# Performance work log

Hardware: AMD Instinct MI355X
Metric: run time of the kernel (lower is better)

## Reference

```python
import jax, jax.numpy as jnp
import numpy as np

MAX_LEN = 150
DIM_HEAD = 64


def setup_inputs() -> dict:
    key = jax.random.key(0)
    kq, kk, kv, kp, km = jax.random.split(key, 5)
    B, H, L, Dh = 4, 16, 1024, DIM_HEAD
    q = jax.random.normal(kq, (B, H, L, Dh), dtype=jnp.float32)
    k = jax.random.normal(kk, (B, H, L, Dh), dtype=jnp.float32)
    v = jax.random.normal(kv, (B, H, L, Dh), dtype=jnp.float32)
    pos_embedding = jax.random.normal(kp, (2 * MAX_LEN + 1, Dh), dtype=jnp.float32)
    mask = jax.random.randint(km, (B, 1, 1, L), 0, 2).astype(bool)
    return {"q": q, "k": k, "v": v, "pos_embedding": pos_embedding, "mask": mask}


def reference(q, k, v, pos_embedding, mask):
    B, H, Lq, Dh = q.shape
    Lk = k.shape[2]
    scale = jnp.asarray(np.sqrt(Dh), dtype=q.dtype)
    # relative position index: clamp(j - i, -max_len, max_len) + max_len - 1
    # (faithful to source, incl. the -1 offset; index -1 wraps to last row in both torch and jax)
    rel = jnp.arange(Lk)[None, :] - jnp.arange(Lq)[:, None]
    rel_idx = jnp.clip(rel, -MAX_LEN, MAX_LEN) + MAX_LEN - 1  # [Lq, Lk]
    R = pos_embedding[rel_idx]  # [Lq, Lk, Dh]
    # relative-position score: q_t @ R^T  ->  [B, H, Lq, Lk]
    rp = jnp.einsum('bhqd,qkd->bhqk', q, R)
    scores = (jnp.einsum('bhqd,bhkd->bhqk', q, k) + rp) / scale
    scores = jnp.where(mask, -jnp.inf, scores)
    attn = jax.nn.softmax(scores, axis=-1)
    return jnp.einsum('bhqk,bhkd->bhqd', attn, v)
```

## Files before the change

kernel.cpp:

```cpp
#include <hip/hip_runtime.h>
#include <math.h>


#define LL 1024
#define DH 64
#define MAXL 150

typedef __attribute__((ext_vector_type(8)))  short    short8;
typedef __attribute__((ext_vector_type(4)))  float    f32x4;
typedef __attribute__((ext_vector_type(16))) float    f32x16;
typedef __attribute__((ext_vector_type(4)))  unsigned u32x4;

union U4S8 { u32x4 u; short8 s; };

__device__ __forceinline__ unsigned f2bf(float f) {
  unsigned u = __float_as_uint(f);
  u += 0x7FFFu + ((u >> 16) & 1u);
  return u >> 16;
}
__device__ __forceinline__ unsigned pkbf(float lo, float hi) {
  return f2bf(lo) | (f2bf(hi) << 16);
}
__device__ __forceinline__ float bf2f(unsigned short s) {
  return __uint_as_float((unsigned)s << 16);
}
__device__ __forceinline__ short8 pack8f(float4 a, float4 b) {
  U4S8 t;
  t.u[0] = pkbf(a.x, a.y); t.u[1] = pkbf(a.z, a.w);
  t.u[2] = pkbf(b.x, b.y); t.u[3] = pkbf(b.z, b.w);
  return t.s;
}
__device__ __forceinline__ int swz(int row, int cb) {
  return row * 128 + (cb ^ ((row & 7) << 4));
}
__device__ __forceinline__ void st_pair(unsigned char* base, int row, int colb,
                                        float a, float b) {
  unsigned u = pkbf(a, b);
  *(unsigned short*)(base + swz(row, colb))     = (unsigned short)u;
  *(unsigned short*)(base + swz(row + 1, colb)) = (unsigned short)(u >> 16);
}
#define KOFF(r) ((((r) & 3)) + 8 * ((r) >> 2))

__global__ __launch_bounds__(256, 2)
void rp_attn32(const float* __restrict__ Q, const float* __restrict__ K,
               const float* __restrict__ V, const float* __restrict__ POS,
               const int* __restrict__ MSK, float* __restrict__ OUT) {
  __shared__ __attribute__((aligned(16))) unsigned short qrs[64][306];
  __shared__ __attribute__((aligned(16))) unsigned char  kv[32768];
  __shared__ __attribute__((aligned(16))) float          mskf[2][64];

  const int tid = threadIdx.x;
  const int F  = blockIdx.x;
  const int gi = F >> 3;
  const int bh = (F & 7) * 8 + (gi >> 4);
  const int i0 = (gi & 15) * 64;
  const int b  = bh >> 4;

  const int wave = tid >> 6, lane = tid & 63;
  const int lo5 = lane & 31, hi = lane >> 5;
  const int qg = wave & 1, kh = wave >> 1;
  const int qloc = qg * 32 + lo5;
  const int irow = i0 + qloc;

  const size_t bo = (size_t)bh * LL * DH;
  const float* qp = Q + bo;
  const float* kp = K + bo;
  const float* vp = V + bo;
  const int*   mrow = MSK + b * LL;

  unsigned char* ksh = kv + kh * 8192;
  unsigned char* vth = kv + 16384 + kh * 8192;

  short8 qB[4];
#pragma unroll
  for (int c = 0; c < 4; ++c) {
    const float* src = qp + (size_t)irow * DH + c * 16 + hi * 8;
    qB[c] = pack8f(*(const float4*)src, *(const float4*)(src + 4));
  }

  for (int tb = kh; tb < 10; tb += 2) {
    int trow = tb * 32 + lo5; if (trow > 300) trow = 300;
    const float* pr = POS + (size_t)trow * DH;
    f32x16 z;
#pragma unroll
    for (int x = 0; x < 16; ++x) z[x] = 0.f;
#pragma unroll
    for (int c = 0; c < 4; ++c) {
      const float* s2 = pr + c * 16 + hi * 8;
      short8 af = pack8f(*(const float4*)s2, *(const float4*)(s2 + 4));
      z = __builtin_amdgcn_mfma_f32_32x32x16_bf16(af, qB[c], z, 0, 0, 0);
    }
#pragma unroll
    for (int rp = 0; rp < 8; ++rp) {
      const int r = rp * 2;
      int tp = KOFF(r) + 4 * hi + 32 * tb;
      if (tp < 306)
        *(unsigned*)(&qrs[qloc][tp]) = pkbf(z[r], z[r + 1]);
    }
  }

  const float SC = 0.18033688011112042f;
  float m2 = -1e30f, lsum = 0.f;
  f32x16 acc0, acc1;
#pragma unroll
  for (int x = 0; x < 16; ++x) { acc0[x] = 0.f; acc1[x] = 0.f; }

  for (int rd = 0; rd < 8; ++rd) {
    __syncthreads();
    {
      const int r = tid >> 2, q4 = tid & 3, r2 = r * 2, rb = q4 * 16;
#pragma unroll
      for (int h = 0; h < 2; ++h) {
        const int j0h = h * 512 + rd * 64;
        const float* ksrc = kp + (size_t)(j0h + r) * DH + q4 * 16;
        float4 k0 = ((const float4*)ksrc)[0], k1 = ((const float4*)ksrc)[1];
        float4 k2 = ((const float4*)ksrc)[2], k3 = ((const float4*)ksrc)[3];
        unsigned char* kb_ = kv + h * 8192;
        *(short8*)(kb_ + swz(r, q4 * 32))      = pack8f(k0, k1);
        *(short8*)(kb_ + swz(r, q4 * 32 + 16)) = pack8f(k2, k3);
        const float* vsrc = vp + (size_t)(j0h + r) * DH + q4 * 16;
        float4 v0 = ((const float4*)vsrc)[0], v1 = ((const float4*)vsrc)[1];
        float4 v2 = ((const float4*)vsrc)[2], v3 = ((const float4*)vsrc)[3];
        unsigned char* vb_ = kv + 16384 + h * 8192;
        st_pair(vb_, rb + 0,  r2, v0.x, v0.y); st_pair(vb_, rb + 2,  r2, v0.z, v0.w);
        st_pair(vb_, rb + 4,  r2, v1.x, v1.y); st_pair(vb_, rb + 6,  r2, v1.z, v1.w);
        st_pair(vb_, rb + 8,  r2, v2.x, v2.y); st_pair(vb_, rb + 10, r2, v2.z, v2.w);
        st_pair(vb_, rb + 12, r2, v3.x, v3.y); st_pair(vb_, rb + 14, r2, v3.z, v3.w);
      }
      if (tid < 128) {
        int h = tid >> 6, kk = tid & 63;
        mskf[h][kk] = mrow[h * 512 + rd * 64 + kk] ? -INFINITY : 0.0f;
      }
    }
    __syncthreads();

    const int j0 = kh * 512 + rd * 64;

    f32x16 st[2];
#pragma unroll
    for (int kb = 0; kb < 2; ++kb) {
      f32x16 z;
#pragma unroll
      for (int x = 0; x < 16; ++x) z[x] = 0.f;
#pragma unroll
      for (int c = 0; c < 4; ++c) {
        short8 kf = *(const short8*)(ksh + swz(kb * 32 + lo5, c * 32 + hi * 16));
        z = __builtin_amdgcn_mfma_f32_32x32x16_bf16(kf, qB[c], z, 0, 0, 0);
      }
      st[kb] = z;
    }

#pragma unroll
    for (int kb = 0; kb < 2; ++kb) {
      const int jb = j0 + kb * 32;
      f32x4 mg[4];
#pragma unroll
      for (int g4 = 0; g4 < 4; ++g4)
        mg[g4] = *(const f32x4*)&mskf[kh][kb * 32 + g4 * 8 + 4 * hi];
      const int relmin = jb - (i0 + qg * 32 + 31);
      const int relmax = jb + 31 - (i0 + qg * 32);
      if (relmin >= MAXL) {
        const float bias = bf2f(qrs[qloc][299]);
#pragma unroll
        for (int r = 0; r < 16; ++r)
          st[kb][r] = (st[kb][r] + bias) * SC + mg[r >> 2][r & 3];
      } else if (relmax <= -MAXL) {
        const float bias = bf2f(qrs[qloc][300]);
#pragma unroll
        for (int r = 0; r < 16; ++r)
          st[kb][r] = (st[kb][r] + bias) * SC + mg[r >> 2][r & 3];
      } else {
#pragma unroll
        for (int r = 0; r < 16; ++r) {
          const int rel = jb + KOFF(r) + 4 * hi - irow;
          const int idx = rel <= -MAXL ? 300 : (rel >= MAXL ? 299 : rel + MAXL - 1);
          st[kb][r] = (st[kb][r] + bf2f(qrs[qloc][idx])) * SC + mg[r >> 2][r & 3];
        }
      }
    }

    f32x16 mx;
#pragma unroll
    for (int r = 0; r < 16; ++r) mx[r] = fmaxf(st[0][r], st[1][r]);
#pragma unroll
    for (int w = 8; w > 0; w >>= 1)
#pragma unroll
      for (int r = 0; r < 8; ++r)
        if (r < w) mx[r] = fmaxf(mx[r], mx[r + w]);
    float tmax = fmaxf(mx[0], __shfl_xor(mx[0], 32));
    const float mnew = fmaxf(m2, tmax);
    const float alpha = exp2f(m2 - mnew);
#pragma unroll
    for (int kb = 0; kb < 2; ++kb)
#pragma unroll
      for (int r = 0; r < 16; ++r) st[kb][r] = exp2f(st[kb][r] - mnew);
    f32x16 sx;
#pragma unroll
    for (int r = 0; r < 16; ++r) sx[r] = st[0][r] + st[1][r];
#pragma unroll
    for (int w = 8; w > 0; w >>= 1)
#pragma unroll
      for (int r = 0; r < 8; ++r)
        if (r < w) sx[r] = sx[r] + sx[r + w];
    const float ps = sx[0] + __shfl_xor(sx[0], 32);
    lsum = lsum * alpha + ps;
    m2 = mnew;
    acc0 *= alpha; acc1 *= alpha;

    short8 pf[4];
#pragma unroll
    for (int ch = 0; ch < 4; ++ch) {
      const int kb = ch >> 1, rb2 = (ch & 1) * 8;
      unsigned a  = pkbf(st[kb][rb2 + 0], st[kb][rb2 + 1]);
      unsigned a2 = pkbf(st[kb][rb2 + 2], st[kb][rb2 + 3]);
      unsigned bb = pkbf(st[kb][rb2 + 4], st[kb][rb2 + 5]);
      unsigned b2 = pkbf(st[kb][rb2 + 6], st[kb][rb2 + 7]);
      unsigned sa  = __shfl_xor(a, 32);
      unsigned sa2 = __shfl_xor(a2, 32);
      unsigned sbb = __shfl_xor(bb, 32);
      unsigned sb2 = __shfl_xor(b2, 32);
      U4S8 t;
      t.u[0] = hi ? sbb : a;
      t.u[1] = hi ? sb2 : a2;
      t.u[2] = hi ? bb  : sa;
      t.u[3] = hi ? b2  : sa2;
      pf[ch] = t.s;
    }

#pragma unroll
    for (int ch = 0; ch < 4; ++ch) {
      short8 vf0 = *(const short8*)(vth + swz(lo5,      ch * 32 + hi * 16));
      short8 vf1 = *(const short8*)(vth + swz(32 + lo5, ch * 32 + hi * 16));
      acc0 = __builtin_amdgcn_mfma_f32_32x32x16_bf16(vf0, pf[ch], acc0, 0, 0, 0);
      acc1 = __builtin_amdgcn_mfma_f32_32x32x16_bf16(vf1, pf[ch], acc1, 0, 0, 0);
    }
  }

  __syncthreads();
  float* mb = (float*)kv;
  if (wave >= 2) {
    float* d = mb + ((wave - 2) * 64 + lane) * 37;
    d[0] = m2; d[1] = lsum;
#pragma unroll
    for (int r = 0; r < 16; ++r) { d[2 + r] = acc0[r]; d[18 + r] = acc1[r]; }
  }
  __syncthreads();
  if (wave < 2) {
    const float* d = mb + (wave * 64 + lane) * 37;
    const float m1 = d[0], l1 = d[1];
    const float mf = fmaxf(m2, m1);
    const float a0 = exp2f(m2 - mf), a1 = exp2f(m1 - mf);
    const float lf = lsum * a0 + l1 * a1;
    const float inv = 1.f / lf;
    float* op = OUT + bo + (size_t)irow * DH;
#pragma unroll
    for (int r = 0; r < 16; ++r) {
      const int d0 = KOFF(r) + 4 * hi;
      op[d0]      = (acc0[r] * a0 + d[2 + r]  * a1) * inv;
      op[d0 + 32] = (acc1[r] * a0 + d[18 + r] * a1) * inv;
    }
  }
}

extern "C" void kernel_launch(void* const* d_in, const int* in_sizes, int n_in,
                              void* d_out, int out_size, void* d_ws, size_t ws_size,
                              hipStream_t stream) {
  const float* q   = (const float*)d_in[0];
  const float* k   = (const float*)d_in[1];
  const float* v   = (const float*)d_in[2];
  const float* pos = (const float*)d_in[3];
  const int*   msk = (const int*)d_in[4];
  float* out = (float*)d_out;

  rp_attn32<<<dim3(1024), dim3(256), 0, stream>>>(q, k, v, pos, msk, out);
}
```

Baseline: 98.67 us.

## Prefetch K/V into registers, use hardware bf16 pack, lazy softmax rescale

Several changes land together. The next K/V tile is loaded from global memory into registers right after the barrier, so the load overlaps the current tile's compute. Software bf16 rounding is replaced with the v_cvt_pk_bf16_f32 instruction. The whole mask row is preloaded into LDS once, and the V transpose store uses a different thread mapping. The online-softmax rescale is skipped unless the running max grows by more than a threshold. In exchange the prefetch adds register pressure, which may hurt occupancy under launch_bounds(256,2), and the lazy rescale leaves probabilities bounded by 2^12 rather than 1 before the bf16 pack.

```diff
diff --git a/kernel.cpp b/kernel.cpp
--- a/kernel.cpp
+++ b/kernel.cpp
@@ -13,21 +13,18 @@
 
 union U4S8 { u32x4 u; short8 s; };
 
-__device__ __forceinline__ unsigned f2bf(float f) {
-  unsigned u = __float_as_uint(f);
-  u += 0x7FFFu + ((u >> 16) & 1u);
-  return u >> 16;
-}
-__device__ __forceinline__ unsigned pkbf(float lo, float hi) {
-  return f2bf(lo) | (f2bf(hi) << 16);
+__device__ __forceinline__ unsigned cvtpk(float lo, float hi) {
+  unsigned r;
+  asm("v_cvt_pk_bf16_f32 %0, %1, %2" : "=v"(r) : "v"(lo), "v"(hi));
+  return r;
 }
 __device__ __forceinline__ float bf2f(unsigned short s) {
   return __uint_as_float((unsigned)s << 16);
 }
 __device__ __forceinline__ short8 pack8f(float4 a, float4 b) {
   U4S8 t;
-  t.u[0] = pkbf(a.x, a.y); t.u[1] = pkbf(a.z, a.w);
-  t.u[2] = pkbf(b.x, b.y); t.u[3] = pkbf(b.z, b.w);
+  t.u[0] = cvtpk(a.x, a.y); t.u[1] = cvtpk(a.z, a.w);
+  t.u[2] = cvtpk(b.x, b.y); t.u[3] = cvtpk(b.z, b.w);
   return t.s;
 }
 __device__ __forceinline__ int swz(int row, int cb) {
@@ -35,7 +32,7 @@
 }
 __device__ __forceinline__ void st_pair(unsigned char* base, int row, int colb,
                                         float a, float b) {
-  unsigned u = pkbf(a, b);
+  unsigned u = cvtpk(a, b);
   *(unsigned short*)(base + swz(row, colb))     = (unsigned short)u;
   *(unsigned short*)(base + swz(row + 1, colb)) = (unsigned short)(u >> 16);
 }
@@ -47,7 +44,7 @@
                const int* __restrict__ MSK, float* __restrict__ OUT) {
   __shared__ __attribute__((aligned(16))) unsigned short qrs[64][306];
   __shared__ __attribute__((aligned(16))) unsigned char  kv[32768];
-  __shared__ __attribute__((aligned(16))) float          mskf[2][64];
+  __shared__ __attribute__((aligned(16))) float          mskf[1024];
 
   const int tid = threadIdx.x;
   const int F  = blockIdx.x;
@@ -62,6 +59,9 @@
   const int qloc = qg * 32 + lo5;
   const int irow = i0 + qloc;
 
+  const int rK = tid >> 2, q4 = tid & 3;
+  const int kkV = tid & 63, dwV = wave;
+
   const size_t bo = (size_t)bh * LL * DH;
   const float* qp = Q + bo;
   const float* kp = K + bo;
@@ -78,6 +78,12 @@
     qB[c] = pack8f(*(const float4*)src, *(const float4*)(src + 4));
   }
 
+#pragma unroll
+  for (int t2 = 0; t2 < 4; ++t2) {
+    const int ix = tid + t2 * 256;
+    mskf[ix] = mrow[ix] ? -INFINITY : 0.0f;
+  }
+
   for (int tb = kh; tb < 10; tb += 2) {
     int trow = tb * 32 + lo5; if (trow > 300) trow = 300;
     const float* pr = POS + (size_t)trow * DH;
@@ -95,7 +101,7 @@
       const int r = rp * 2;
       int tp = KOFF(r) + 4 * hi + 32 * tb;
       if (tp < 306)
-        *(unsigned*)(&qrs[qloc][tp]) = pkbf(z[r], z[r + 1]);
+        *(unsigned*)(&qrs[qloc][tp]) = cvtpk(z[r], z[r + 1]);
     }
   }
 
@@ -105,34 +111,40 @@
 #pragma unroll
   for (int x = 0; x < 16; ++x) { acc0[x] = 0.f; acc1[x] = 0.f; }
 
+  float4 kreg[2][4], vreg[2][4];
+  auto LOADT = [&](int rdx) {
+#pragma unroll
+    for (int h = 0; h < 2; ++h) {
+      const float* ksrc = kp + (size_t)(h * 512 + rdx * 64 + rK) * DH + q4 * 16;
+#pragma unroll
+      for (int i = 0; i < 4; ++i) kreg[h][i] = ((const float4*)ksrc)[i];
+      const float* vsrc = vp + (size_t)(h * 512 + rdx * 64 + kkV) * DH + dwV * 16;
+#pragma unroll
+      for (int i = 0; i < 4; ++i) vreg[h][i] = ((const float4*)vsrc)[i];
+    }
+  };
+  LOADT(0);
+
   for (int rd = 0; rd < 8; ++rd) {
     __syncthreads();
-    {
-      const int r = tid >> 2, q4 = tid & 3, r2 = r * 2, rb = q4 * 16;
-#pragma unroll
-      for (int h = 0; h < 2; ++h) {
-        const int j0h = h * 512 + rd * 64;
-        const float* ksrc = kp + (size_t)(j0h + r) * DH + q4 * 16;
-        float4 k0 = ((const float4*)ksrc)[0], k1 = ((const float4*)ksrc)[1];
-        float4 k2 = ((const float4*)ksrc)[2], k3 = ((const float4*)ksrc)[3];
-        unsigned char* kb_ = kv + h * 8192;
-        *(short8*)(kb_ + swz(r, q4 * 32))      = pack8f(k0, k1);
-        *(short8*)(kb_ + swz(r, q4 * 32 + 16)) = pack8f(k2, k3);
-        const float* vsrc = vp + (size_t)(j0h + r) * DH + q4 * 16;
-        float4 v0 = ((const float4*)vsrc)[0], v1 = ((const float4*)vsrc)[1];
-        float4 v2 = ((const float4*)vsrc)[2], v3 = ((const float4*)vsrc)[3];
-        unsigned char* vb_ = kv + 16384 + h * 8192;
-        st_pair(vb_, rb + 0,  r2, v0.x, v0.y); st_pair(vb_, rb + 2,  r2, v0.z, v0.w);
-        st_pair(vb_, rb + 4,  r2, v1.x, v1.y); st_pair(vb_, rb + 6,  r2, v1.z, v1.w);
-        st_pair(vb_, rb + 8,  r2, v2.x, v2.y); st_pair(vb_, rb + 10, r2, v2.z, v2.w);
-        st_pair(vb_, rb + 12, r2, v3.x, v3.y); st_pair(vb_, rb + 14, r2, v3.z, v3.w);
-      }
-      if (tid < 128) {
-        int h = tid >> 6, kk = tid & 63;
-        mskf[h][kk] = mrow[h * 512 + rd * 64 + kk] ? -INFINITY : 0.0f;
-      }
+#pragma unroll
+    for (int h = 0; h < 2; ++h) {
+      unsigned char* kb_ = kv + h * 8192;
+      *(short8*)(kb_ + swz(rK, q4 * 32))      = pack8f(kreg[h][0], kreg[h][1]);
+      *(short8*)(kb_ + swz(rK, q4 * 32 + 16)) = pack8f(kreg[h][2], kreg[h][3]);
+      unsigned char* vb_ = kv + 16384 + h * 8192;
+      const int db = dwV * 16, cb2 = kkV * 2;
+      st_pair(vb_, db + 0,  cb2, vreg[h][0].x, vreg[h][0].y);
+      st_pair(vb_, db + 2,  cb2, vreg[h][0].z, vreg[h][0].w);
+      st_pair(vb_, db + 4,  cb2, vreg[h][1].x, vreg[h][1].y);
+      st_pair(vb_, db + 6,  cb2, vreg[h][1].z, vreg[h][1].w);
+      st_pair(vb_, db + 8,  cb2, vreg[h][2].x, vreg[h][2].y);
+      st_pair(vb_, db + 10, cb2, vreg[h][2].z, vreg[h][2].w);
+      st_pair(vb_, db + 12, cb2, vreg[h][3].x, vreg[h][3].y);
+      st_pair(vb_, db + 14, cb2, vreg[h][3].z, vreg[h][3].w);
     }
     __syncthreads();
+    if (rd < 7) LOADT(rd + 1);
 
     const int j0 = kh * 512 + rd * 64;
 
@@ -156,7 +168,7 @@
       f32x4 mg[4];
 #pragma unroll
       for (int g4 = 0; g4 < 4; ++g4)
-        mg[g4] = *(const f32x4*)&mskf[kh][kb * 32 + g4 * 8 + 4 * hi];
+        mg[g4] = *(const f32x4*)&mskf[jb + g4 * 8 + 4 * hi];
       const int relmin = jb - (i0 + qg * 32 + 31);
       const int relmax = jb + 31 - (i0 + qg * 32);
       if (relmin >= MAXL) {
@@ -187,13 +199,18 @@
 #pragma unroll
       for (int r = 0; r < 8; ++r)
         if (r < w) mx[r] = fmaxf(mx[r], mx[r + w]);
-    float tmax = fmaxf(mx[0], __shfl_xor(mx[0], 32));
-    const float mnew = fmaxf(m2, tmax);
-    const float alpha = exp2f(m2 - mnew);
+    const float tmax = fmaxf(mx[0], __shfl_xor(mx[0], 32));
+    if (!__all(tmax - m2 <= 12.0f)) {
+      const float mnew = fmaxf(m2, tmax);
+      const float alpha = exp2f(m2 - mnew);
+      lsum *= alpha;
+      acc0 *= alpha; acc1 *= alpha;
+      m2 = mnew;
+    }
 #pragma unroll
     for (int kb = 0; kb < 2; ++kb)
 #pragma unroll
-      for (int r = 0; r < 16; ++r) st[kb][r] = exp2f(st[kb][r] - mnew);
+      for (int r = 0; r < 16; ++r) st[kb][r] = exp2f(st[kb][r] - m2);
     f32x16 sx;
 #pragma unroll
     for (int r = 0; r < 16; ++r) sx[r] = st[0][r] + st[1][r];
@@ -202,19 +219,16 @@
 #pragma unroll
       for (int r = 0; r < 8; ++r)
         if (r < w) sx[r] = sx[r] + sx[r + w];
-    const float ps = sx[0] + __shfl_xor(sx[0], 32);
-    lsum = lsum * alpha + ps;
-    m2 = mnew;
-    acc0 *= alpha; acc1 *= alpha;
+    lsum += sx[0] + __shfl_xor(sx[0], 32);
 
     short8 pf[4];
 #pragma unroll
     for (int ch = 0; ch < 4; ++ch) {
       const int kb = ch >> 1, rb2 = (ch & 1) * 8;
-      unsigned a  = pkbf(st[kb][rb2 + 0], st[kb][rb2 + 1]);
-      unsigned a2 = pkbf(st[kb][rb2 + 2], st[kb][rb2 + 3]);
-      unsigned bb = pkbf(st[kb][rb2 + 4], st[kb][rb2 + 5]);
-      unsigned b2 = pkbf(st[kb][rb2 + 6], st[kb][rb2 + 7]);
+      unsigned a  = cvtpk(st[kb][rb2 + 0], st[kb][rb2 + 1]);
+      unsigned a2 = cvtpk(st[kb][rb2 + 2], st[kb][rb2 + 3]);
+      unsigned bb = cvtpk(st[kb][rb2 + 4], st[kb][rb2 + 5]);
+      unsigned b2 = cvtpk(st[kb][rb2 + 6], st[kb][rb2 + 7]);
       unsigned sa  = __shfl_xor(a, 32);
       unsigned sa2 = __shfl_xor(a2, 32);
       unsigned sbb = __shfl_xor(bb, 32);
```

Result: faster. 95.13 us (-3.6%).
